# Optimization experiments

Hardware: AMD Instinct MI355X
Metric: run time of the kernel (lower is better)

Reference implementation:

```python
import jax, jax.numpy as jnp
import numpy as np

B, C, H, W = 2, 512, 64, 64
NH = 8
EPS = 1e-5


def setup_inputs() -> dict:
    key = jax.random.key(0)
    ks = jax.random.split(key, 4)
    s_in = 1.0 / np.sqrt(C)
    x = jax.random.normal(ks[0], (B, C, H, W), dtype=jnp.float32)
    qkv_w = jax.random.normal(ks[1], (3 * C, C), dtype=jnp.float32) * s_in
    qkv_b = jnp.zeros((3 * C,), dtype=jnp.float32)
    out_w = jax.random.normal(ks[2], (C, C), dtype=jnp.float32) * s_in
    out_b = jnp.zeros((C,), dtype=jnp.float32)
    ln_g = jnp.ones((C,), dtype=jnp.float32)
    ln_b = jnp.zeros((C,), dtype=jnp.float32)
    return {"x": x, "qkv_w": qkv_w, "qkv_b": qkv_b, "out_w": out_w,
            "out_b": out_b, "ln_g": ln_g, "ln_b": ln_b, "num_heads": NH}


def reference(x, qkv_w, qkv_b, out_w, out_b, ln_g, ln_b, num_heads):
    b, c, h, w = x.shape
    n = h * w
    hd = c // num_heads
    scale = hd ** -0.5

    # flatten spatial: [B, N, C]
    tokens = x.reshape(b, c, n).transpose(0, 2, 1)

    # fused QKV projection
    qkv = tokens @ qkv_w.T + qkv_b            # [B, N, 3C]
    q, k, v = jnp.split(qkv, 3, axis=-1)

    def heads(t):  # [B, N, C] -> [B, H, N, D]
        return t.reshape(b, n, num_heads, hd).transpose(0, 2, 1, 3)

    q, k, v = heads(q), heads(k), heads(v)

    # naive full attention (materializes [B, H, N, N] as in the original)
    scores = jnp.einsum('bhqd,bhkd->bhqk', q, k) * scale
    attn = jax.nn.softmax(scores, axis=-1)
    out = jnp.einsum('bhqk,bhkd->bhqd', attn, v)  # [B, H, N, D]

    out = out.transpose(0, 2, 1, 3).reshape(b, n, c)
    attended = out @ out_w.T + out_b          # [B, N, C]

    # residual + LayerNorm over channels
    res = attended + tokens
    mean = jnp.mean(res, axis=-1, keepdims=True)
    var = jnp.var(res, axis=-1, keepdims=True)
    y = (res - mean) * jax.lax.rsqrt(var + EPS) * ln_g + ln_b

    return y.transpose(0, 2, 1).reshape(b, c, h, w)
```

## Files before the change

### kernel.cpp

```cpp
#include <hip/hip_runtime.h>

#define BATCH 2
#define CH    512
#define NTOK  4096
#define NH    8
#define HD    64
#define MTOT  (BATCH*NTOK)

typedef __attribute__((ext_vector_type(8))) __bf16 bf16x8;
typedef __attribute__((ext_vector_type(4))) float  f32x4;
typedef __attribute__((ext_vector_type(4))) unsigned short u16x4;

static __device__ __forceinline__ f32x4 mfma16(bf16x8 a, bf16x8 b, f32x4 c) {
  return __builtin_amdgcn_mfma_f32_16x16x32_bf16(a, b, c, 0, 0, 0);
}

static __device__ __forceinline__ unsigned short f2bf(float f) {
  unsigned int u = __float_as_uint(f);
  u += 0x7fffu + ((u >> 16) & 1u);
  return (unsigned short)(u >> 16);
}

static __device__ __forceinline__ void gload_lds16(const unsigned short* g, unsigned short* l) {
  __builtin_amdgcn_global_load_lds((const __attribute__((address_space(1))) void*)g,
                                   (__attribute__((address_space(3))) void*)l, 16, 0, 0);
}

#define QSC 0.18033688011112042f

__global__ __launch_bounds__(256) void k_transpose(const float* __restrict__ x,
                                                   unsigned short* __restrict__ tokB) {
  __shared__ float tile[32][33];
  int b  = blockIdx.z;
  int n0 = blockIdx.x * 32;
  int c0 = blockIdx.y * 32;
  int tx = threadIdx.x & 31, ty = threadIdx.x >> 5;
#pragma unroll
  for (int i = 0; i < 4; i++) {
    int c = c0 + ty + 8 * i;
    tile[ty + 8 * i][tx] = x[((size_t)b * CH + c) * NTOK + n0 + tx];
  }
  __syncthreads();
#pragma unroll
  for (int i = 0; i < 4; i++) {
    int n = n0 + ty + 8 * i;
    int c = c0 + tx;
    tokB[((size_t)b * NTOK + n) * CH + c] = f2bf(tile[tx][ty + 8 * i]);
  }
}

__global__ __launch_bounds__(256) void k_castw(const float* __restrict__ w1,
                                               const float* __restrict__ w2,
                                               unsigned short* __restrict__ o1,
                                               unsigned short* __restrict__ o2) {
  int i = blockIdx.x * 256 + threadIdx.x;
  if (i < 3 * CH * CH) o1[i] = f2bf(w1[i]);
  else o2[i - 3 * CH * CH] = f2bf(w2[i - 3 * CH * CH]);
}

#define BK 64

static __device__ __forceinline__ void stage_g(const unsigned short* __restrict__ src,
                                               size_t row0, int k0,
                                               unsigned short* __restrict__ lds,
                                               int wid, int lane) {
  int sub = lane >> 3;
  int ch  = (lane & 7) ^ sub;
#pragma unroll
  for (int i = 0; i < 4; i++) {
    int rbase = 32 * wid + 8 * i;
    gload_lds16(&src[(row0 + rbase + sub) * 512 + k0 + ch * 8], &lds[rbase * BK]);
  }
}

static __device__ __forceinline__ bf16x8 frag_ld(const unsigned short* __restrict__ lds,
                                                 int row, int ks, int lane) {
  int ch = ((ks << 2) + (lane >> 4)) ^ (row & 7);
  return *reinterpret_cast<const bf16x8*>(&lds[row * BK + ch * 8]);
}

__global__ __launch_bounds__(256) void k_gemm_qkv(const unsigned short* __restrict__ A,
                                                  const unsigned short* __restrict__ W,
                                                  const float* __restrict__ bias,
                                                  unsigned short* __restrict__ qb,
                                                  unsigned short* __restrict__ kb,
                                                  unsigned short* __restrict__ vt) {
  __shared__ unsigned short lsA[128 * BK];
  __shared__ unsigned short lsB[128 * BK];
  int bm0 = blockIdx.x * 128;
  int bn0 = blockIdx.y * 128;
  int tid = threadIdx.x, lane = tid & 63, wid = tid >> 6;
  int wm = wid >> 1, wn = wid & 1;

  f32x4 acc[4][4];
  f32x4 zz = {0.f, 0.f, 0.f, 0.f};
#pragma unroll
  for (int i = 0; i < 4; i++)
#pragma unroll
    for (int j = 0; j < 4; j++) acc[i][j] = zz;

  for (int k0 = 0; k0 < 512; k0 += BK) {
    stage_g(A, (size_t)bm0, k0, lsA, wid, lane);
    stage_g(W, (size_t)bn0, k0, lsB, wid, lane);
    __syncthreads();
#pragma unroll
    for (int ks = 0; ks < 2; ks++) {
      bf16x8 af[4], bfr[4];
#pragma unroll
      for (int t = 0; t < 4; t++) {
        af[t]  = frag_ld(lsA, wm * 64 + t * 16 + (lane & 15), ks, lane);
        bfr[t] = frag_ld(lsB, wn * 64 + t * 16 + (lane & 15), ks, lane);
      }
#pragma unroll
      for (int mt = 0; mt < 4; mt++)
#pragma unroll
        for (int nt = 0; nt < 4; nt++) acc[mt][nt] = mfma16(af[mt], bfr[nt], acc[mt][nt]);
    }
    __syncthreads();
  }
#pragma unroll
  for (int nt = 0; nt < 4; nt++) {
    int j = bn0 + wn * 64 + nt * 16 + (lane & 15);
    float bj = bias[j];
    int which = j >> 9;
    int cp = j & 511;
    int h = cp >> 6, d = cp & 63;
    if (which == 2) {
#pragma unroll
      for (int mt = 0; mt < 4; mt++) {
        int m = bm0 + wm * 64 + mt * 16 + 4 * (lane >> 4);
        int b = m >> 12, n = m & 4095;
        u16x4 pk;
#pragma unroll
        for (int r = 0; r < 4; r++) pk[r] = f2bf(acc[mt][nt][r] + bj);
        *reinterpret_cast<u16x4*>(&vt[((size_t)((b * NH + h) * HD + d)) * NTOK + n]) = pk;
      }
    } else {
      unsigned short* dst = (which == 0) ? qb : kb;
      float sc = (which == 0) ? QSC : 1.0f;
#pragma unroll
      for (int mt = 0; mt < 4; mt++) {
#pragma unroll
        for (int r = 0; r < 4; r++) {
          int m = bm0 + wm * 64 + mt * 16 + 4 * (lane >> 4) + r;
          int b = m >> 12, n = m & 4095;
          dst[(((size_t)(b * NH + h) * NTOK + n) << 6) + d] = f2bf((acc[mt][nt][r] + bj) * sc);
        }
      }
    }
  }
}

#define KVB 64
#define NT  (NTOK / KVB)

static __device__ __forceinline__ void stage_kv(const unsigned short* __restrict__ Kp,
                                                const unsigned short* __restrict__ Vp,
                                                unsigned short* __restrict__ lk,
                                                unsigned short* __restrict__ lv,
                                                int kv0, int wid, int srow, int schunk) {
#pragma unroll
  for (int i = 0; i < 2; i++) {
    int rbase = 16 * wid + 8 * i;
    int row = rbase + srow;
    gload_lds16(&Kp[((size_t)(kv0 + row) << 6) + (schunk << 3)], &lk[rbase << 6]);
    gload_lds16(&Vp[(size_t)row * NTOK + kv0 + (schunk << 3)], &lv[rbase << 6]);
  }
}

static __device__ __forceinline__ void softmax_pack(f32x4* s, unsigned short* __restrict__ P,
                                                    int g, int lr) {
#pragma unroll
  for (int ct = 0; ct < 4; ct++) {
    s[ct][0] = __builtin_exp2f(s[ct][0]);
    s[ct][1] = __builtin_exp2f(s[ct][1]);
    s[ct][2] = __builtin_exp2f(s[ct][2]);
    s[ct][3] = __builtin_exp2f(s[ct][3]);
  }
  int l7 = lr & 7;
#pragma unroll
  for (int ct = 0; ct < 4; ct++) {
    unsigned int lo, hi;
    asm("v_cvt_pk_bf16_f32 %0, %1, %2" : "=v"(lo) : "v"(s[ct][0]), "v"(s[ct][1]));
    asm("v_cvt_pk_bf16_f32 %0, %1, %2" : "=v"(hi) : "v"(s[ct][2]), "v"(s[ct][3]));
    uint2 pk; pk.x = lo; pk.y = hi;
    int chunk = ((ct << 1) + (g >> 1)) ^ l7;
    *reinterpret_cast<uint2*>(&P[(lr << 6) + (chunk << 3) + ((g & 1) << 2)]) = pk;
  }
}

static __device__ __forceinline__ void attn_tile(const unsigned short* __restrict__ lk,
                                                 const unsigned short* __restrict__ lv,
                                                 unsigned short* __restrict__ P0,
                                                 unsigned short* __restrict__ P1,
                                                 const bf16x8 qf[2][2],
                                                 f32x4* oacc0, f32x4* oacc1,
                                                 f32x4& lacc0, f32x4& lacc1,
                                                 bf16x8 onesf, int g, int lr) {
  f32x4 zz = {0.f, 0.f, 0.f, 0.f};
  int l7 = lr & 7;
  bf16x8 kf[4][2];
#pragma unroll
  for (int ct = 0; ct < 4; ct++)
#pragma unroll
    for (int ks = 0; ks < 2; ks++)
      kf[ct][ks] = *reinterpret_cast<const bf16x8*>(
          &lk[((ct * 16 + lr) << 6) + ((((ks << 2) + g) ^ l7) << 3)]);
  f32x4 s0[4], s1[4];
#pragma unroll
  for (int ct = 0; ct < 4; ct++) {
    s0[ct] = zz; s1[ct] = zz;
#pragma unroll
    for (int ks = 0; ks < 2; ks++) {
      s0[ct] = mfma16(kf[ct][ks], qf[0][ks], s0[ct]);
      s1[ct] = mfma16(kf[ct][ks], qf[1][ks], s1[ct]);
    }
  }
  bf16x8 vf[4][2];
#pragma unroll
  for (int dt = 0; dt < 4; dt++)
#pragma unroll
    for (int ks = 0; ks < 2; ks++)
      vf[dt][ks] = *reinterpret_cast<const bf16x8*>(
          &lv[((dt * 16 + lr) << 6) + ((((ks << 2) + g) ^ l7) << 3)]);
  softmax_pack(s0, P0, g, lr);
  softmax_pack(s1, P1, g, lr);
#pragma unroll
  for (int ks = 0; ks < 2; ks++) {
    bf16x8 pf0 = *reinterpret_cast<const bf16x8*>(
        &P0[(lr << 6) + ((((ks << 2) + g) ^ l7) << 3)]);
    bf16x8 pf1 = *reinterpret_cast<const bf16x8*>(
        &P1[(lr << 6) + ((((ks << 2) + g) ^ l7) << 3)]);
#pragma unroll
    for (int dt = 0; dt < 4; dt++) {
      oacc0[dt] = mfma16(pf0, vf[dt][ks], oacc0[dt]);
      oacc1[dt] = mfma16(pf1, vf[dt][ks], oacc1[dt]);
    }
    lacc0 = mfma16(pf0, onesf, lacc0);
    lacc1 = mfma16(pf1, onesf, lacc1);
  }
}

__global__ __launch_bounds__(256, 2) void k_attn(const unsigned short* __restrict__ Q,
                                                 const unsigned short* __restrict__ K,
                                                 const unsigned short* __restrict__ Vt,
                                                 unsigned short* __restrict__ O) {
  __shared__ unsigned short lsK[2][KVB * 64];
  __shared__ unsigned short lsV[2][64 * KVB];
  __shared__ unsigned short lsp[4][2][16 * KVB];
  int gid = blockIdx.y * 32 + blockIdx.x;
  int vv  = (gid & 7) * 64 + (gid >> 3);
  int bh  = vv >> 5;
  int tid = threadIdx.x, lane = tid & 63, wid = tid >> 6;
  int g = lane >> 4, lr = lane & 15;
  int qw = (vv & 31) * 128 + wid * 32;
  const unsigned short* Qp = Q + (size_t)bh * NTOK * HD;
  const unsigned short* Kp = K + (size_t)bh * NTOK * HD;
  const unsigned short* Vp = Vt + (size_t)bh * HD * NTOK;
  unsigned short* P0 = &lsp[wid][0][0];
  unsigned short* P1 = &lsp[wid][1][0];
  unsigned short* K0 = &lsK[0][0]; unsigned short* K1 = &lsK[1][0];
  unsigned short* V0 = &lsV[0][0]; unsigned short* V1 = &lsV[1][0];

  int srow = lane >> 3;
  int schunk = (lane & 7) ^ srow;

  union { unsigned short u[8]; bf16x8 v; } ou;
#pragma unroll
  for (int i = 0; i < 8; i++) ou.u[i] = 0x3F80;
  bf16x8 onesf = ou.v;

  bf16x8 qf[2][2];
#pragma unroll
  for (int sq = 0; sq < 2; sq++)
#pragma unroll
    for (int ks = 0; ks < 2; ks++)
      qf[sq][ks] = *reinterpret_cast<const bf16x8*>(
          &Qp[(size_t)(qw + sq * 16 + lr) * HD + ks * 32 + 8 * g]);

  f32x4 zz = {0.f, 0.f, 0.f, 0.f};
  f32x4 oacc0[4] = {zz, zz, zz, zz};
  f32x4 oacc1[4] = {zz, zz, zz, zz};
  f32x4 lacc0 = zz, lacc1 = zz;

  stage_kv(Kp, Vp, K0, V0, 0, wid, srow, schunk);
  __syncthreads();

  for (int t = 0; t < NT; t += 2) {
    stage_kv(Kp, Vp, K1, V1, (t + 1) * KVB, wid, srow, schunk);
    attn_tile(K0, V0, P0, P1, qf, oacc0, oacc1, lacc0, lacc1, onesf, g, lr);
    __syncthreads();
    if (t + 2 < NT) stage_kv(Kp, Vp, K0, V0, (t + 2) * KVB, wid, srow, schunk);
    attn_tile(K1, V1, P0, P1, qf, oacc0, oacc1, lacc0, lacc1, onesf, g, lr);
    __syncthreads();
  }
  int b2 = bh >> 3, h = bh & 7;
#pragma unroll
  for (int sq = 0; sq < 2; sq++) {
    f32x4* oacc = sq ? oacc1 : oacc0;
    f32x4  lacc = sq ? lacc1 : lacc0;
#pragma unroll
    for (int r = 0; r < 4; r++) {
      float inv = 1.0f / lacc[r];
      int n = qw + sq * 16 + 4 * g + r;
#pragma unroll
      for (int dt = 0; dt < 4; dt++) {
        int d = dt * 16 + lr;
        O[((size_t)(b2 * NTOK + n)) * CH + h * HD + d] = f2bf(oacc[dt][r] * inv);
      }
    }
  }
}

__global__ __launch_bounds__(256) void k_gemm_out(const unsigned short* __restrict__ A,
                                                  const unsigned short* __restrict__ W,
                                                  const float* __restrict__ bias,
                                                  const unsigned short* __restrict__ tokB,
                                                  float* __restrict__ res) {
  __shared__ unsigned short lsA[128 * BK];
  __shared__ unsigned short lsB[128 * BK];
  int bm0 = blockIdx.x * 128;
  int bn0 = blockIdx.y * 128;
  int tid = threadIdx.x, lane = tid & 63, wid = tid >> 6;
  int wm = wid >> 1, wn = wid & 1;

  f32x4 acc[4][4];
  f32x4 zz = {0.f, 0.f, 0.f, 0.f};
#pragma unroll
  for (int i = 0; i < 4; i++)
#pragma unroll
    for (int j = 0; j < 4; j++) acc[i][j] = zz;

  for (int k0 = 0; k0 < 512; k0 += BK) {
    stage_g(A, (size_t)bm0, k0, lsA, wid, lane);
    stage_g(W, (size_t)bn0, k0, lsB, wid, lane);
    __syncthreads();
#pragma unroll
    for (int ks = 0; ks < 2; ks++) {
      bf16x8 af[4], bfr[4];
#pragma unroll
      for (int t = 0; t < 4; t++) {
        af[t]  = frag_ld(lsA, wm * 64 + t * 16 + (lane & 15), ks, lane);
        bfr[t] = frag_ld(lsB, wn * 64 + t * 16 + (lane & 15), ks, lane);
      }
#pragma unroll
      for (int mt = 0; mt < 4; mt++)
#pragma unroll
        for (int nt = 0; nt < 4; nt++) acc[mt][nt] = mfma16(af[mt], bfr[nt], acc[mt][nt]);
    }
    __syncthreads();
  }
#pragma unroll
  for (int nt = 0; nt < 4; nt++) {
    int j = bn0 + wn * 64 + nt * 16 + (lane & 15);
    float bj = bias[j];
#pragma unroll
    for (int mt = 0; mt < 4; mt++) {
#pragma unroll
      for (int r = 0; r < 4; r++) {
        int m = bm0 + wm * 64 + mt * 16 + 4 * (lane >> 4) + r;
        size_t idx = (size_t)m * CH + j;
        float tk = __uint_as_float((unsigned int)tokB[idx] << 16);
        res[idx] = acc[mt][nt][r] + bj + tk;
      }
    }
  }
}

__global__ __launch_bounds__(256) void k_ln(const float* __restrict__ res,
                                            const float* __restrict__ g,
                                            const float* __restrict__ bb,
                                            float* __restrict__ y) {
  __shared__ float smean[64], srstd[64];
  int m0 = blockIdx.x * 64;
  int tid = threadIdx.x, lane = tid & 63, wid = tid >> 6;
  for (int t = 0; t < 16; t++) {
    int idx = wid * 16 + t;
    const float* row = res + (size_t)(m0 + idx) * CH;
    float s = 0.f, ss = 0.f;
#pragma unroll
    for (int i = 0; i < 8; i++) {
      float v = row[lane + 64 * i];
      s += v; ss += v * v;
    }
#pragma unroll
    for (int off = 1; off < 64; off <<= 1) {
      s += __shfl_xor(s, off);
      ss += __shfl_xor(ss, off);
    }
    if (lane == 0) {
      float mean = s * (1.0f / CH);
      float var = ss * (1.0f / CH) - mean * mean;
      smean[idx] = mean;
      srstd[idx] = rsqrtf(var + 1e-5f);
    }
  }
  __syncthreads();
  int b = m0 >> 12, n0 = m0 & 4095;
  int tn = tid & 63;
  int cq = tid >> 6;
  float mn = smean[tn], rs = srstd[tn];
  const float* rrow = res + (size_t)(m0 + tn) * CH;
  for (int c = cq; c < CH; c += 4) {
    float v = (rrow[c] - mn) * rs * g[c] + bb[c];
    y[((size_t)b * CH + c) * NTOK + n0 + tn] = v;
  }
}

extern "C" void kernel_launch(void* const* d_in, const int* in_sizes, int n_in,
                              void* d_out, int out_size, void* d_ws, size_t ws_size,
                              hipStream_t stream) {
  const float* x    = (const float*)d_in[0];
  const float* qkvw = (const float*)d_in[1];
  const float* qkvb = (const float*)d_in[2];
  const float* outw = (const float*)d_in[3];
  const float* outb = (const float*)d_in[4];
  const float* lng  = (const float*)d_in[5];
  const float* lnb  = (const float*)d_in[6];
  float* y = (float*)d_out;

  const size_t NC = (size_t)MTOT * CH;
  char* ws = (char*)d_ws;
  size_t off = 0;
  auto nxt = [&](size_t bytes) -> void* {
    void* p = ws + off;
    off += (bytes + 255) & ~(size_t)255;
    return p;
  };
  unsigned short* tokB = (unsigned short*)nxt(NC * 2);
  unsigned short* wqkv = (unsigned short*)nxt((size_t)3 * CH * CH * 2);
  unsigned short* wout = (unsigned short*)nxt((size_t)CH * CH * 2);
  unsigned short* qb   = (unsigned short*)nxt(NC * 2);
  unsigned short* kb   = (unsigned short*)nxt(NC * 2);
  unsigned short* vt   = (unsigned short*)nxt(NC * 2);
  unsigned short* ao   = (unsigned short*)nxt(NC * 2);
  float*          resb = (float*)nxt(NC * 4);
  if (off > ws_size) return;

  k_transpose<<<dim3(NTOK / 32, CH / 32, BATCH), 256, 0, stream>>>(x, tokB);
  k_castw<<<(4 * CH * CH) / 256, 256, 0, stream>>>(qkvw, outw, wqkv, wout);
  k_gemm_qkv<<<dim3(MTOT / 128, (3 * CH) / 128), 256, 0, stream>>>(tokB, wqkv, qkvb, qb, kb, vt);
  k_attn<<<dim3(32, 16), 256, 0, stream>>>(qb, kb, vt, ao);
  k_gemm_out<<<dim3(MTOT / 128, CH / 128), 256, 0, stream>>>(ao, wout, outb, tokB, resb);
  k_ln<<<MTOT / 64, 256, 0, stream>>>(resb, lng, lnb, y);
}
```

Baseline: 196.3 us.

## Keep softmax probabilities in registers by permuting K row order

Reorders which K tokens each MFMA column tile covers, with a matching swizzle in LDS staging, so the S-tile output layout lines up directly with the A-operand layout of the PV MFMA. The exponentiated scores are packed to bf16 in registers and fed straight into the PV and row-sum MFMAs, removing the per-wave LDS round trip (store P, then reload) and the LDS buffer that held P. The K staging swizzle and read addressing change to stay bank-conflict free under the new row permutation, and register pressure may rise slightly.

```diff
diff --git a/kernel.cpp b/kernel.cpp
--- a/kernel.cpp
+++ b/kernel.cpp
@@ -158,54 +158,37 @@
                                                 const unsigned short* __restrict__ Vp,
                                                 unsigned short* __restrict__ lk,
                                                 unsigned short* __restrict__ lv,
-                                                int kv0, int wid, int srow, int schunk) {
+                                                int kv0, int wid, int lane) {
+  int sub = lane >> 3;
+  int c7  = lane & 7;
 #pragma unroll
   for (int i = 0; i < 2; i++) {
     int rbase = 16 * wid + 8 * i;
-    int row = rbase + srow;
-    gload_lds16(&Kp[((size_t)(kv0 + row) << 6) + (schunk << 3)], &lk[rbase << 6]);
-    gload_lds16(&Vp[(size_t)row * NTOK + kv0 + (schunk << 3)], &lv[rbase << 6]);
-  }
-}
-
-static __device__ __forceinline__ void softmax_pack(f32x4* s, unsigned short* __restrict__ P,
-                                                    int g, int lr) {
-#pragma unroll
-  for (int ct = 0; ct < 4; ct++) {
-    s[ct][0] = __builtin_exp2f(s[ct][0]);
-    s[ct][1] = __builtin_exp2f(s[ct][1]);
-    s[ct][2] = __builtin_exp2f(s[ct][2]);
-    s[ct][3] = __builtin_exp2f(s[ct][3]);
-  }
-  int l7 = lr & 7;
-#pragma unroll
-  for (int ct = 0; ct < 4; ct++) {
-    unsigned int lo, hi;
-    asm("v_cvt_pk_bf16_f32 %0, %1, %2" : "=v"(lo) : "v"(s[ct][0]), "v"(s[ct][1]));
-    asm("v_cvt_pk_bf16_f32 %0, %1, %2" : "=v"(hi) : "v"(s[ct][2]), "v"(s[ct][3]));
-    uint2 pk; pk.x = lo; pk.y = hi;
-    int chunk = ((ct << 1) + (g >> 1)) ^ l7;
-    *reinterpret_cast<uint2*>(&P[(lr << 6) + (chunk << 3) + ((g & 1) << 2)]) = pk;
+    int row = rbase + sub;
+    int fk = (sub & 3) | (i << 2);
+    gload_lds16(&Kp[((size_t)(kv0 + row) << 6) + ((c7 ^ fk) << 3)], &lk[rbase << 6]);
+    gload_lds16(&Vp[(size_t)row * NTOK + kv0 + ((c7 ^ sub) << 3)], &lv[rbase << 6]);
   }
 }
 
 static __device__ __forceinline__ void attn_tile(const unsigned short* __restrict__ lk,
                                                  const unsigned short* __restrict__ lv,
-                                                 unsigned short* __restrict__ P0,
-                                                 unsigned short* __restrict__ P1,
                                                  const bf16x8 qf[2][2],
                                                  f32x4* oacc0, f32x4* oacc1,
                                                  f32x4& lacc0, f32x4& lacc1,
                                                  bf16x8 onesf, int g, int lr) {
   f32x4 zz = {0.f, 0.f, 0.f, 0.f};
   int l7 = lr & 7;
+  int tbase = 8 * (lr >> 2) + (lr & 3);
+  int kc0 = ((g ^ l7) << 3);
+  int kc1 = (((4 + g) ^ l7) << 3);
   bf16x8 kf[4][2];
 #pragma unroll
-  for (int ct = 0; ct < 4; ct++)
-#pragma unroll
-    for (int ks = 0; ks < 2; ks++)
-      kf[ct][ks] = *reinterpret_cast<const bf16x8*>(
-          &lk[((ct * 16 + lr) << 6) + ((((ks << 2) + g) ^ l7) << 3)]);
+  for (int ct = 0; ct < 4; ct++) {
+    int t = tbase + 4 * (ct >> 1) + 32 * (ct & 1);
+    kf[ct][0] = *reinterpret_cast<const bf16x8*>(&lk[(t << 6) + kc0]);
+    kf[ct][1] = *reinterpret_cast<const bf16x8*>(&lk[(t << 6) + kc1]);
+  }
   f32x4 s0[4], s1[4];
 #pragma unroll
   for (int ct = 0; ct < 4; ct++) {
@@ -218,27 +201,43 @@
   }
   bf16x8 vf[4][2];
 #pragma unroll
-  for (int dt = 0; dt < 4; dt++)
-#pragma unroll
-    for (int ks = 0; ks < 2; ks++)
-      vf[dt][ks] = *reinterpret_cast<const bf16x8*>(
-          &lv[((dt * 16 + lr) << 6) + ((((ks << 2) + g) ^ l7) << 3)]);
-  softmax_pack(s0, P0, g, lr);
-  softmax_pack(s1, P1, g, lr);
-#pragma unroll
-  for (int ks = 0; ks < 2; ks++) {
-    bf16x8 pf0 = *reinterpret_cast<const bf16x8*>(
-        &P0[(lr << 6) + ((((ks << 2) + g) ^ l7) << 3)]);
-    bf16x8 pf1 = *reinterpret_cast<const bf16x8*>(
-        &P1[(lr << 6) + ((((ks << 2) + g) ^ l7) << 3)]);
-#pragma unroll
-    for (int dt = 0; dt < 4; dt++) {
-      oacc0[dt] = mfma16(pf0, vf[dt][ks], oacc0[dt]);
-      oacc1[dt] = mfma16(pf1, vf[dt][ks], oacc1[dt]);
-    }
-    lacc0 = mfma16(pf0, onesf, lacc0);
-    lacc1 = mfma16(pf1, onesf, lacc1);
-  }
+  for (int dt = 0; dt < 4; dt++) {
+    vf[dt][0] = *reinterpret_cast<const bf16x8*>(&lv[((dt * 16 + lr) << 6) + kc0]);
+    vf[dt][1] = *reinterpret_cast<const bf16x8*>(&lv[((dt * 16 + lr) << 6) + kc1]);
+  }
+#pragma unroll
+  for (int ct = 0; ct < 4; ct++) {
+#pragma unroll
+    for (int r = 0; r < 4; r++) {
+      s0[ct][r] = __builtin_exp2f(s0[ct][r]);
+      s1[ct][r] = __builtin_exp2f(s1[ct][r]);
+    }
+  }
+  unsigned int w0[4][2], w1[4][2];
+#pragma unroll
+  for (int ct = 0; ct < 4; ct++) {
+    asm("v_cvt_pk_bf16_f32 %0, %1, %2" : "=v"(w0[ct][0]) : "v"(s0[ct][0]), "v"(s0[ct][1]));
+    asm("v_cvt_pk_bf16_f32 %0, %1, %2" : "=v"(w0[ct][1]) : "v"(s0[ct][2]), "v"(s0[ct][3]));
+    asm("v_cvt_pk_bf16_f32 %0, %1, %2" : "=v"(w1[ct][0]) : "v"(s1[ct][0]), "v"(s1[ct][1]));
+    asm("v_cvt_pk_bf16_f32 %0, %1, %2" : "=v"(w1[ct][1]) : "v"(s1[ct][2]), "v"(s1[ct][3]));
+  }
+  union U { unsigned int w[4]; bf16x8 v; };
+  U a0, a1, b0, b1;
+  a0.w[0] = w0[0][0]; a0.w[1] = w0[0][1]; a0.w[2] = w0[2][0]; a0.w[3] = w0[2][1];
+  a1.w[0] = w0[1][0]; a1.w[1] = w0[1][1]; a1.w[2] = w0[3][0]; a1.w[3] = w0[3][1];
+  b0.w[0] = w1[0][0]; b0.w[1] = w1[0][1]; b0.w[2] = w1[2][0]; b0.w[3] = w1[2][1];
+  b1.w[0] = w1[1][0]; b1.w[1] = w1[1][1]; b1.w[2] = w1[3][0]; b1.w[3] = w1[3][1];
+#pragma unroll
+  for (int dt = 0; dt < 4; dt++) {
+    oacc0[dt] = mfma16(a0.v, vf[dt][0], oacc0[dt]);
+    oacc0[dt] = mfma16(a1.v, vf[dt][1], oacc0[dt]);
+    oacc1[dt] = mfma16(b0.v, vf[dt][0], oacc1[dt]);
+    oacc1[dt] = mfma16(b1.v, vf[dt][1], oacc1[dt]);
+  }
+  lacc0 = mfma16(a0.v, onesf, lacc0);
+  lacc0 = mfma16(a1.v, onesf, lacc0);
+  lacc1 = mfma16(b0.v, onesf, lacc1);
+  lacc1 = mfma16(b1.v, onesf, lacc1);
 }
 
 __global__ __launch_bounds__(256, 2) void k_attn(const unsigned short* __restrict__ Q,
@@ -247,7 +246,6 @@
                                                  unsigned short* __restrict__ O) {
   __shared__ unsigned short lsK[2][KVB * 64];
   __shared__ unsigned short lsV[2][64 * KVB];
-  __shared__ unsigned short lsp[4][2][16 * KVB];
   int gid = blockIdx.y * 32 + blockIdx.x;
   int vv  = (gid & 7) * 64 + (gid >> 3);
   int bh  = vv >> 5;
@@ -257,13 +255,8 @@
   const unsigned short* Qp = Q + (size_t)bh * NTOK * HD;
   const unsigned short* Kp = K + (size_t)bh * NTOK * HD;
   const unsigned short* Vp = Vt + (size_t)bh * HD * NTOK;
-  unsigned short* P0 = &lsp[wid][0][0];
-  unsigned short* P1 = &lsp[wid][1][0];
   unsigned short* K0 = &lsK[0][0]; unsigned short* K1 = &lsK[1][0];
   unsigned short* V0 = &lsV[0][0]; unsigned short* V1 = &lsV[1][0];
-
-  int srow = lane >> 3;
-  int schunk = (lane & 7) ^ srow;
 
   union { unsigned short u[8]; bf16x8 v; } ou;
 #pragma unroll
@@ -283,15 +276,15 @@
   f32x4 oacc1[4] = {zz, zz, zz, zz};
   f32x4 lacc0 = zz, lacc1 = zz;
 
-  stage_kv(Kp, Vp, K0, V0, 0, wid, srow, schunk);
+  stage_kv(Kp, Vp, K0, V0, 0, wid, lane);
   __syncthreads();
 
   for (int t = 0; t < NT; t += 2) {
-    stage_kv(Kp, Vp, K1, V1, (t + 1) * KVB, wid, srow, schunk);
-    attn_tile(K0, V0, P0, P1, qf, oacc0, oacc1, lacc0, lacc1, onesf, g, lr);
-    __syncthreads();
-    if (t + 2 < NT) stage_kv(Kp, Vp, K0, V0, (t + 2) * KVB, wid, srow, schunk);
-    attn_tile(K1, V1, P0, P1, qf, oacc0, oacc1, lacc0, lacc1, onesf, g, lr);
+    stage_kv(Kp, Vp, K1, V1, (t + 1) * KVB, wid, lane);
+    attn_tile(K0, V0, qf, oacc0, oacc1, lacc0, lacc1, onesf, g, lr);
+    __syncthreads();
+    if (t + 2 < NT) stage_kv(Kp, Vp, K0, V0, (t + 2) * KVB, wid, lane);
+    attn_tile(K1, V1, qf, oacc0, oacc1, lacc0, lacc1, onesf, g, lr);
     __syncthreads();
   }
   int b2 = bh >> 3, h = bh & 7;
```

Result: faster. 184.5 us (-6.0%).
